# Performance work log

Hardware: AMD Instinct MI355X
Metric: run time of the kernel (lower is better)

Reference implementation:

```python
import jax, jax.numpy as jnp
import numpy as np

ALPHA = 0.4
EPS = 1e-5


def setup_inputs() -> dict:
    key = jax.random.key(0)
    features = jax.random.normal(key, (32, 1024, 512), dtype=jnp.float32)
    return {"features": features}


def reference(features):
    B, dim, M = features.shape
    # x_pow2 = x @ x^T / (2M), shape [B, dim, dim]
    x_pow2 = jnp.einsum('bdm,bem->bde', features, features) / (2.0 * M)
    # I_M.bmm(x_pow2*I) broadcasts the diagonal along rows; (x_pow2*I).bmm(I_M) along cols
    diag = jnp.diagonal(x_pow2, axis1=1, axis2=2)  # [B, dim]
    dcov = diag[:, None, :] + diag[:, :, None] - 2.0 * x_pow2
    dcov = jnp.maximum(dcov, 0.0)
    dcov = jnp.power(dcov + EPS, ALPHA)
    # double-centering: the ones/dim matmuls are exactly row/col/total means
    row_mean = jnp.mean(dcov, axis=2, keepdims=True)   # dcov.bmm(I_M/dim)
    col_mean = jnp.mean(dcov, axis=1, keepdims=True)   # (I_M/dim).bmm(dcov)
    tot_mean = jnp.mean(dcov, axis=(1, 2), keepdims=True)
    out = dcov - row_mean - col_mean + tot_mean        # [B, dim, dim]
    # triuvec: upper-triangular (incl. diagonal) entries, row-major order
    idx = np.nonzero(np.triu(np.ones((dim, dim), dtype=np.float32)).reshape(-1))[0]
    return out.reshape(B, dim * dim)[:, idx]
```

## Files before the change

### kernel.cpp

```cpp
#include <hip/hip_runtime.h>
#include <hip/hip_bf16.h>

#define B_ 32
#define D_ 1024
#define M_ 512
#define OUTROW 524800
#define ALPHA_ 0.4f
#define EPS_ 1e-5f

typedef __bf16 bf16x8 __attribute__((ext_vector_type(8)));
typedef __bf16 bf16x4 __attribute__((ext_vector_type(4)));
typedef float f32x4 __attribute__((ext_vector_type(4)));

__global__ __launch_bounds__(256) void prep_kernel(
    const float* __restrict__ feat, __bf16* __restrict__ featbf,
    float* __restrict__ diag, float* __restrict__ rowsum,
    float* __restrict__ totals)
{
    if (blockIdx.x < 128) {
        rowsum[blockIdx.x * 256 + threadIdx.x] = 0.0f;
        if (blockIdx.x == 0 && threadIdx.x < B_) totals[threadIdx.x] = 0.0f;
    }

    const int w = threadIdx.x >> 6, l = threadIdx.x & 63;
    const int row = blockIdx.x * 4 + w;
    const float4* fp = (const float4*)(feat + (size_t)row * M_);
    float4 v0 = fp[l * 2];
    float4 v1 = fp[l * 2 + 1];
    bf16x8 h;
    h[0] = (__bf16)v0.x; h[1] = (__bf16)v0.y; h[2] = (__bf16)v0.z; h[3] = (__bf16)v0.w;
    h[4] = (__bf16)v1.x; h[5] = (__bf16)v1.y; h[6] = (__bf16)v1.z; h[7] = (__bf16)v1.w;
    *(bf16x8*)(featbf + (size_t)row * M_ + l * 8) = h;
    float s = v0.x*v0.x + v0.y*v0.y + v0.z*v0.z + v0.w*v0.w
            + v1.x*v1.x + v1.y*v1.y + v1.z*v1.z + v1.w*v1.w;
    #pragma unroll
    for (int off = 32; off; off >>= 1) s += __shfl_down(s, off);
    if (l == 0) diag[row] = s * (1.0f / (2.0f * M_));
}

__global__ __launch_bounds__(256, 3) void gram_kernel(
    const __bf16* __restrict__ feat, const float* __restrict__ diag,
    float* __restrict__ out, __bf16* __restrict__ pbuf,
    float* __restrict__ rowsum, float* __restrict__ totals, int useP)
{
    __shared__ __bf16 As[3][512 * 8];
    __shared__ __bf16 Bs[3][512 * 8];

    const int t = threadIdx.x;
    const int w = t >> 6, l = t & 63;
    const int quad = l >> 4, l15 = l & 15;

    const int L = blockIdx.x;
    const int xcd = L & 7;
    const int slot = L >> 3;
    const int b = xcd + 8 * (slot / 36);
    int u = slot % 36, ti = 0;
    while (u >= 8 - ti) { u -= 8 - ti; ti++; }
    const int tj = ti + u;
    const bool diagTile = (ti == tj);

    const __bf16* Ab = feat + (size_t)b * (D_ * M_) + (size_t)ti * 128 * M_;
    const __bf16* Bb = feat + (size_t)b * (D_ * M_) + (size_t)tj * 128 * M_;

    const int wm = w >> 1, wn = w & 1;

    const int gi0 = ti * 128 + wm * 64;
    const int gj0 = tj * 128 + wn * 64;
    const float* diagB = diag + b * D_;
    float di[4][4], dj[4];
    #pragma unroll
    for (int mi = 0; mi < 4; ++mi)
        #pragma unroll
        for (int r = 0; r < 4; ++r)
            di[mi][r] = diagB[gi0 + mi * 16 + quad * 4 + r];
    #pragma unroll
    for (int nj = 0; nj < 4; ++nj)
        dj[nj] = diagB[gj0 + nj * 16 + l15];

    f32x4 acc[4][4] = {};

    auto stage = [&](int s, int sb) {
        const int koff = s * 32;
        #pragma unroll
        for (int it = 0; it < 2; ++it) {
            const int idx = it * 256 + t;
            const int row = idx >> 2;
            const int cg = (idx & 3) ^ ((row >> 1) & 3);
            const __bf16* ga = Ab + row * M_ + koff + cg * 8;
            const __bf16* gb = Bb + row * M_ + koff + cg * 8;
            __builtin_amdgcn_global_load_lds(
                (const __attribute__((address_space(1))) void*)ga,
                (__attribute__((address_space(3))) void*)(&As[sb][(it * 256 + w * 64) * 8]),
                16, 0, 0);
            __builtin_amdgcn_global_load_lds(
                (const __attribute__((address_space(1))) void*)gb,
                (__attribute__((address_space(3))) void*)(&Bs[sb][(it * 256 + w * 64) * 8]),
                16, 0, 0);
        }
    };

    stage(0, 0);
    stage(1, 1);
    int rb = 0, sn = 2;
    for (int k0 = 0; k0 < 16; ++k0) {
        if (k0 < 15) asm volatile("s_waitcnt vmcnt(4)" ::: "memory");
        else         asm volatile("s_waitcnt vmcnt(0)" ::: "memory");
        __builtin_amdgcn_s_barrier();
        __builtin_amdgcn_sched_barrier(0);
        if (k0 + 2 < 16) stage(k0 + 2, sn);

        bf16x8 af[4], bfr[4];
        #pragma unroll
        for (int mi = 0; mi < 4; ++mi) {
            const int row = wm * 64 + mi * 16 + l15;
            af[mi] = *(const bf16x8*)(&As[rb][(row * 4 + (quad ^ ((row >> 1) & 3))) * 8]);
        }
        #pragma unroll
        for (int nj = 0; nj < 4; ++nj) {
            const int row = wn * 64 + nj * 16 + l15;
            bfr[nj] = *(const bf16x8*)(&Bs[rb][(row * 4 + (quad ^ ((row >> 1) & 3))) * 8]);
        }
        __builtin_amdgcn_s_setprio(1);
        #pragma unroll
        for (int mi = 0; mi < 4; ++mi)
            #pragma unroll
            for (int nj = 0; nj < 4; ++nj)
                acc[mi][nj] = __builtin_amdgcn_mfma_f32_16x16x32_bf16(
                    af[mi], bfr[nj], acc[mi][nj], 0, 0, 0);
        __builtin_amdgcn_s_setprio(0);
        rb = (rb == 2) ? 0 : rb + 1;
        sn = (sn == 2) ? 0 : sn + 1;
    }

    float* outB = out + (size_t)b * OUTROW;
    __bf16* pB = pbuf + (size_t)b * OUTROW;
    float rs[4][4] = {};
    float cs[4] = {};
    float wt = 0.f;
    const float invK = 1.0f / 512.0f;

    #pragma unroll
    for (int mi = 0; mi < 4; ++mi) {
        #pragma unroll
        for (int nj = 0; nj < 4; ++nj) {
            const f32x4 a = acc[mi][nj];
            const int j = gj0 + nj * 16 + l15;
            #pragma unroll
            for (int r = 0; r < 4; ++r) {
                const int i = gi0 + mi * 16 + quad * 4 + r;
                float d = di[mi][r] + dj[nj] - a[r] * invK;
                if (i == j) d = 0.0f;
                d = fmaxf(d, 0.0f);
                const float p = __builtin_exp2f(ALPHA_ * __builtin_log2f(d + EPS_));
                rs[mi][r] += p;
                cs[nj] += p;
                wt += p;
                if (!diagTile || j >= i) {
                    const size_t idx =
                        (size_t)i * D_ - ((size_t)i * (i + 1)) / 2 + j;
                    if (useP) pB[idx] = (__bf16)p;
                    else      outB[idx] = p;
                }
            }
        }
    }

    #pragma unroll
    for (int mi = 0; mi < 4; ++mi) {
        #pragma unroll
        for (int r = 0; r < 4; ++r) {
            float v = rs[mi][r];
            v += __shfl_xor(v, 1); v += __shfl_xor(v, 2);
            v += __shfl_xor(v, 4); v += __shfl_xor(v, 8);
            if (l15 == 0)
                unsafeAtomicAdd(&rowsum[b * D_ + gi0 + mi * 16 + quad * 4 + r], v);
        }
    }
    if (!diagTile) {
        #pragma unroll
        for (int nj = 0; nj < 4; ++nj) {
            float v = cs[nj];
            v += __shfl_xor(v, 16); v += __shfl_xor(v, 32);
            if (quad == 0)
                unsafeAtomicAdd(&rowsum[b * D_ + gj0 + nj * 16 + l15], v);
        }
    }
    float v = wt;
    #pragma unroll
    for (int off = 32; off; off >>= 1) v += __shfl_down(v, off);
    if (l == 0) unsafeAtomicAdd(&totals[b], diagTile ? v : 2.0f * v);
}

__global__ __launch_bounds__(256) void center_kernel(
    float* __restrict__ out, const __bf16* __restrict__ pbuf,
    const float* __restrict__ rowsum, const float* __restrict__ totals,
    int useP)
{
    __shared__ float rs[D_];
    const int b = blockIdx.y;
    const int tid = threadIdx.x;

    {
        const float4* src = (const float4*)(rowsum + b * D_);
        float4 v = src[tid];
        rs[tid * 4 + 0] = v.x * (1.0f / D_);
        rs[tid * 4 + 1] = v.y * (1.0f / D_);
        rs[tid * 4 + 2] = v.z * (1.0f / D_);
        rs[tid * 4 + 3] = v.w * (1.0f / D_);
    }
    __syncthreads();

    const float tm = totals[b] * (1.0f / ((float)D_ * (float)D_));
    float* outB = out + (size_t)b * OUTROW;
    const __bf16* pBb = pbuf + (size_t)b * OUTROW;

    #pragma unroll
    for (int h = 0; h < 2; ++h) {
        const int i = h ? (D_ - 1 - (int)blockIdx.x) : (int)blockIdx.x;
        const float rmi = rs[i];
        const size_t base = (size_t)i * D_ - ((size_t)i * (i + 1)) / 2;
        float* row = outB + base;
        const __bf16* prow = pBb + base;

        const int mis = (int)((base + i) & 3);
        int jA = i + ((4 - mis) & 3);
        if (jA > D_) jA = D_;
        const int head = jA - i;
        const int rem = D_ - jA;
        const int body4 = rem >> 2;
        const int tail = rem & 3;

        if (useP) {
            if (tid < head) {
                const int j = i + tid;
                row[j] = (float)prow[j] - rmi - rs[j] + tm;
            } else if (tid < head + tail) {
                const int j = D_ - tail + (tid - head);
                row[j] = (float)prow[j] - rmi - rs[j] + tm;
            }
            for (int v = tid; v < body4; v += 256) {
                const int j = jA + v * 4;
                bf16x4 pv = *(const bf16x4*)(prow + j);
                float4 x;
                x.x = (float)pv[0] - rmi - rs[j + 0] + tm;
                x.y = (float)pv[1] - rmi - rs[j + 1] + tm;
                x.z = (float)pv[2] - rmi - rs[j + 2] + tm;
                x.w = (float)pv[3] - rmi - rs[j + 3] + tm;
                *(float4*)(row + j) = x;
            }
        } else {
            if (tid < head) {
                const int j = i + tid;
                row[j] = row[j] - rmi - rs[j] + tm;
            } else if (tid < head + tail) {
                const int j = D_ - tail + (tid - head);
                row[j] = row[j] - rmi - rs[j] + tm;
            }
            for (int v = tid; v < body4; v += 256) {
                const int j = jA + v * 4;
                float4 x = *(float4*)(row + j);
                x.x = x.x - rmi - rs[j + 0] + tm;
                x.y = x.y - rmi - rs[j + 1] + tm;
                x.z = x.z - rmi - rs[j + 2] + tm;
                x.w = x.w - rmi - rs[j + 3] + tm;
                *(float4*)(row + j) = x;
            }
        }
    }
}

extern "C" void kernel_launch(void* const* d_in, const int* in_sizes, int n_in,
                              void* d_out, int out_size, void* d_ws, size_t ws_size,
                              hipStream_t stream) {
    const float* feat = (const float*)d_in[0];
    float* out = (float*)d_out;

    char* ws = (char*)d_ws;
    __bf16* featbf = (__bf16*)ws;
    float* diag    = (float*)(ws + 33554432);
    float* rowsum  = (float*)(ws + 33554432 + 131072);
    float* totals  = (float*)(ws + 33554432 + 262144);
    __bf16* pbuf   = (__bf16*)(ws + 33554432 + 262144 + 128);

    const size_t need = 33554432ull + 262144ull + 128ull + (size_t)OUTROW * 2 * B_;
    const int useP = (ws_size >= need) ? 1 : 0;

    prep_kernel<<<dim3((B_ * D_) / 4), dim3(256), 0, stream>>>(feat, featbf, diag,
                                                               rowsum, totals);
    gram_kernel<<<dim3(36 * B_), dim3(256), 0, stream>>>(featbf, diag, out, pbuf,
                                                         rowsum, totals, useP);
    center_kernel<<<dim3(D_ / 2, B_), dim3(256), 0, stream>>>(out, pbuf, rowsum,
                                                              totals, useP);
}
```

Before: 205.5 us.

## Fuse bf16 conversion and diagonal norms into gram kernel via register staging

Removes the separate prep kernel. The gram kernel now reads fp32 features directly into registers through a three-deep prefetch, converts them to bf16, writes them to double-buffered LDS, and accumulates the squared row norms used for the diagonal. This avoids writing and re-reading a bf16 copy of the features and saves a launch, but each tile re-reads fp32 data (twice the bytes, loaded redundantly across tiles) and does the conversion ALU work inside the GEMM loop. Occupancy drops from 3 to 2 blocks per SIMD because of the extra registers, and the rowsum/totals zeroing moves to a hipMemsetAsync call.

```diff
diff --git a/kernel.cpp b/kernel.cpp
--- a/kernel.cpp
+++ b/kernel.cpp
@@ -12,39 +12,15 @@
 typedef __bf16 bf16x4 __attribute__((ext_vector_type(4)));
 typedef float f32x4 __attribute__((ext_vector_type(4)));
 
-__global__ __launch_bounds__(256) void prep_kernel(
-    const float* __restrict__ feat, __bf16* __restrict__ featbf,
-    float* __restrict__ diag, float* __restrict__ rowsum,
-    float* __restrict__ totals)
-{
-    if (blockIdx.x < 128) {
-        rowsum[blockIdx.x * 256 + threadIdx.x] = 0.0f;
-        if (blockIdx.x == 0 && threadIdx.x < B_) totals[threadIdx.x] = 0.0f;
-    }
-
-    const int w = threadIdx.x >> 6, l = threadIdx.x & 63;
-    const int row = blockIdx.x * 4 + w;
-    const float4* fp = (const float4*)(feat + (size_t)row * M_);
-    float4 v0 = fp[l * 2];
-    float4 v1 = fp[l * 2 + 1];
-    bf16x8 h;
-    h[0] = (__bf16)v0.x; h[1] = (__bf16)v0.y; h[2] = (__bf16)v0.z; h[3] = (__bf16)v0.w;
-    h[4] = (__bf16)v1.x; h[5] = (__bf16)v1.y; h[6] = (__bf16)v1.z; h[7] = (__bf16)v1.w;
-    *(bf16x8*)(featbf + (size_t)row * M_ + l * 8) = h;
-    float s = v0.x*v0.x + v0.y*v0.y + v0.z*v0.z + v0.w*v0.w
-            + v1.x*v1.x + v1.y*v1.y + v1.z*v1.z + v1.w*v1.w;
-    #pragma unroll
-    for (int off = 32; off; off >>= 1) s += __shfl_down(s, off);
-    if (l == 0) diag[row] = s * (1.0f / (2.0f * M_));
-}
-
-__global__ __launch_bounds__(256, 3) void gram_kernel(
-    const __bf16* __restrict__ feat, const float* __restrict__ diag,
+__global__ __launch_bounds__(256, 2) void gram_kernel(
+    const float* __restrict__ feat,
     float* __restrict__ out, __bf16* __restrict__ pbuf,
     float* __restrict__ rowsum, float* __restrict__ totals, int useP)
 {
-    __shared__ __bf16 As[3][512 * 8];
-    __shared__ __bf16 Bs[3][512 * 8];
+    __shared__ __bf16 As[2][512 * 8];
+    __shared__ __bf16 Bs[2][512 * 8];
+    __shared__ float dshA[128];
+    __shared__ float dshB[128];
 
     const int t = threadIdx.x;
     const int w = t >> 6, l = t & 63;
@@ -59,56 +35,76 @@
     const int tj = ti + u;
     const bool diagTile = (ti == tj);
 
-    const __bf16* Ab = feat + (size_t)b * (D_ * M_) + (size_t)ti * 128 * M_;
-    const __bf16* Bb = feat + (size_t)b * (D_ * M_) + (size_t)tj * 128 * M_;
+    const float* Af = feat + (size_t)b * (D_ * M_) + (size_t)ti * 128 * M_;
+    const float* Bf = feat + (size_t)b * (D_ * M_) + (size_t)tj * 128 * M_;
 
     const int wm = w >> 1, wn = w & 1;
 
-    const int gi0 = ti * 128 + wm * 64;
-    const int gj0 = tj * 128 + wn * 64;
-    const float* diagB = diag + b * D_;
-    float di[4][4], dj[4];
-    #pragma unroll
-    for (int mi = 0; mi < 4; ++mi)
-        #pragma unroll
-        for (int r = 0; r < 4; ++r)
-            di[mi][r] = diagB[gi0 + mi * 16 + quad * 4 + r];
-    #pragma unroll
-    for (int nj = 0; nj < 4; ++nj)
-        dj[nj] = diagB[gj0 + nj * 16 + l15];
+    const int r0 = t >> 2;
+    const int r1 = 64 + r0;
+    const int sl = t & 3;
+    const int cg = sl ^ ((r0 >> 1) & 3);
+    const float* gA0 = Af + (size_t)r0 * M_ + cg * 8;
+    const float* gA1 = Af + (size_t)r1 * M_ + cg * 8;
+    const float* gB0 = Bf + (size_t)r0 * M_ + cg * 8;
+    const float* gB1 = Bf + (size_t)r1 * M_ + cg * 8;
 
     f32x4 acc[4][4] = {};
-
-    auto stage = [&](int s, int sb) {
-        const int koff = s * 32;
-        #pragma unroll
-        for (int it = 0; it < 2; ++it) {
-            const int idx = it * 256 + t;
-            const int row = idx >> 2;
-            const int cg = (idx & 3) ^ ((row >> 1) & 3);
-            const __bf16* ga = Ab + row * M_ + koff + cg * 8;
-            const __bf16* gb = Bb + row * M_ + koff + cg * 8;
-            __builtin_amdgcn_global_load_lds(
-                (const __attribute__((address_space(1))) void*)ga,
-                (__attribute__((address_space(3))) void*)(&As[sb][(it * 256 + w * 64) * 8]),
-                16, 0, 0);
-            __builtin_amdgcn_global_load_lds(
-                (const __attribute__((address_space(1))) void*)gb,
-                (__attribute__((address_space(3))) void*)(&Bs[sb][(it * 256 + w * 64) * 8]),
-                16, 0, 0);
-        }
-    };
-
-    stage(0, 0);
-    stage(1, 1);
-    int rb = 0, sn = 2;
-    for (int k0 = 0; k0 < 16; ++k0) {
-        if (k0 < 15) asm volatile("s_waitcnt vmcnt(4)" ::: "memory");
-        else         asm volatile("s_waitcnt vmcnt(0)" ::: "memory");
+    float4 rg[3][8];
+    float dA0 = 0.f, dA1 = 0.f, dB0 = 0.f, dB1 = 0.f;
+
+#define ISSUE(S, KS) {                                   \
+    const int ko = (KS) * 32;                            \
+    rg[S][0] = *(const float4*)(gA0 + ko);               \
+    rg[S][1] = *(const float4*)(gA0 + ko + 4);           \
+    rg[S][2] = *(const float4*)(gA1 + ko);               \
+    rg[S][3] = *(const float4*)(gA1 + ko + 4);           \
+    rg[S][4] = *(const float4*)(gB0 + ko);               \
+    rg[S][5] = *(const float4*)(gB0 + ko + 4);           \
+    rg[S][6] = *(const float4*)(gB1 + ko);               \
+    rg[S][7] = *(const float4*)(gB1 + ko + 4); }
+
+#define CVT8(H, VA, VB)                                                        \
+    H[0]=(__bf16)VA.x; H[1]=(__bf16)VA.y; H[2]=(__bf16)VA.z; H[3]=(__bf16)VA.w;\
+    H[4]=(__bf16)VB.x; H[5]=(__bf16)VB.y; H[6]=(__bf16)VB.z; H[7]=(__bf16)VB.w;
+
+#define SQ8(VA, VB) (VA.x*VA.x + VA.y*VA.y + VA.z*VA.z + VA.w*VA.w +           \
+                     VB.x*VB.x + VB.y*VB.y + VB.z*VB.z + VB.w*VB.w)
+
+#define CVW(S, SB) {                                     \
+    float4 va, vb; bf16x8 h;                             \
+    va = rg[S][0]; vb = rg[S][1];                        \
+    CVT8(h, va, vb)                                      \
+    *(bf16x8*)(&As[SB][(r0 * 4 + sl) * 8]) = h;          \
+    dA0 += SQ8(va, vb);                                  \
+    va = rg[S][2]; vb = rg[S][3];                        \
+    CVT8(h, va, vb)                                      \
+    *(bf16x8*)(&As[SB][(r1 * 4 + sl) * 8]) = h;          \
+    dA1 += SQ8(va, vb);                                  \
+    va = rg[S][4]; vb = rg[S][5];                        \
+    CVT8(h, va, vb)                                      \
+    *(bf16x8*)(&Bs[SB][(r0 * 4 + sl) * 8]) = h;          \
+    dB0 += SQ8(va, vb);                                  \
+    va = rg[S][6]; vb = rg[S][7];                        \
+    CVT8(h, va, vb)                                      \
+    *(bf16x8*)(&Bs[SB][(r1 * 4 + sl) * 8]) = h;          \
+    dB1 += SQ8(va, vb); }
+
+    ISSUE(0, 0);
+    ISSUE(1, 1);
+    ISSUE(2, 2);
+    asm volatile("s_waitcnt vmcnt(16)" ::: "memory");
+    CVW(0, 0);
+
+    #pragma unroll
+    for (int e = 0; e < 16; ++e) {
+        asm volatile("s_waitcnt lgkmcnt(0)" ::: "memory");
         __builtin_amdgcn_s_barrier();
         __builtin_amdgcn_sched_barrier(0);
-        if (k0 + 2 < 16) stage(k0 + 2, sn);
-
+
+        if (e + 3 < 16) ISSUE(e % 3, e + 3);
+
+        const int rb = e & 1;
         bf16x8 af[4], bfr[4];
         #pragma unroll
         for (int mi = 0; mi < 4; ++mi) {
@@ -128,9 +124,37 @@
                 acc[mi][nj] = __builtin_amdgcn_mfma_f32_16x16x32_bf16(
                     af[mi], bfr[nj], acc[mi][nj], 0, 0, 0);
         __builtin_amdgcn_s_setprio(0);
-        rb = (rb == 2) ? 0 : rb + 1;
-        sn = (sn == 2) ? 0 : sn + 1;
-    }
+
+        if (e + 1 < 16) {
+            if (e + 3 < 16)      asm volatile("s_waitcnt vmcnt(16)" ::: "memory");
+            else if (e + 2 < 16) asm volatile("s_waitcnt vmcnt(8)"  ::: "memory");
+            else                 asm volatile("s_waitcnt vmcnt(0)"  ::: "memory");
+            CVW((e + 1) % 3, (e + 1) & 1);
+        }
+    }
+
+    dA0 += __shfl_xor(dA0, 1); dA0 += __shfl_xor(dA0, 2);
+    dA1 += __shfl_xor(dA1, 1); dA1 += __shfl_xor(dA1, 2);
+    dB0 += __shfl_xor(dB0, 1); dB0 += __shfl_xor(dB0, 2);
+    dB1 += __shfl_xor(dB1, 1); dB1 += __shfl_xor(dB1, 2);
+    if (sl == 0) {
+        const float inv2M = 1.0f / (2.0f * M_);
+        dshA[r0] = dA0 * inv2M; dshA[r1] = dA1 * inv2M;
+        dshB[r0] = dB0 * inv2M; dshB[r1] = dB1 * inv2M;
+    }
+    __syncthreads();
+
+    const int gi0 = ti * 128 + wm * 64;
+    const int gj0 = tj * 128 + wn * 64;
+    float di[4][4], dj[4];
+    #pragma unroll
+    for (int mi = 0; mi < 4; ++mi)
+        #pragma unroll
+        for (int r = 0; r < 4; ++r)
+            di[mi][r] = dshA[wm * 64 + mi * 16 + quad * 4 + r];
+    #pragma unroll
+    for (int nj = 0; nj < 4; ++nj)
+        dj[nj] = dshB[wn * 64 + nj * 16 + l15];
 
     float* outB = out + (size_t)b * OUTROW;
     __bf16* pB = pbuf + (size_t)b * OUTROW;
@@ -276,18 +300,19 @@
     float* out = (float*)d_out;
 
     char* ws = (char*)d_ws;
-    __bf16* featbf = (__bf16*)ws;
-    float* diag    = (float*)(ws + 33554432);
-    float* rowsum  = (float*)(ws + 33554432 + 131072);
-    float* totals  = (float*)(ws + 33554432 + 262144);
-    __bf16* pbuf   = (__bf16*)(ws + 33554432 + 262144 + 128);
-
-    const size_t need = 33554432ull + 262144ull + 128ull + (size_t)OUTROW * 2 * B_;
+    __bf16* pbuf  = (__bf16*)ws;
+    float* rowsum = (float*)(ws + 33587200);
+    float* totals = (float*)(ws + 33587200 + 131072);
+
+    const size_t need = 33587200ull + 131072ull + 128ull;
     const int useP = (ws_size >= need) ? 1 : 0;
-
-    prep_kernel<<<dim3((B_ * D_) / 4), dim3(256), 0, stream>>>(feat, featbf, diag,
-                                                               rowsum, totals);
-    gram_kernel<<<dim3(36 * B_), dim3(256), 0, stream>>>(featbf, diag, out, pbuf,
+    if (!useP) {
+        rowsum = (float*)ws;
+        totals = (float*)(ws + 131072);
+    }
+
+    (void)hipMemsetAsync(rowsum, 0, 131072 + 128, stream);
+    gram_kernel<<<dim3(36 * B_), dim3(256), 0, stream>>>(feat, out, pbuf,
                                                          rowsum, totals, useP);
     center_kernel<<<dim3(D_ / 2, B_), dim3(256), 0, stream>>>(out, pbuf, rowsum,
                                                               totals, useP);
```

Result: slower. 222.4 us (+8.2%).
